# Performance work log

Measured on AMD Instinct MI355X. Metric: run time of the kernel, lower is better.

Reference implementation:

```python
import jax, jax.numpy as jnp
import numpy as np

NUM_HEADS = 16

def setup_inputs() -> dict:
    key = jax.random.key(0)
    k1, k2, k3 = jax.random.split(key, 3)
    B, T, C = 4, 2048, 2048
    x = jax.random.normal(k1, (B, T, C), dtype=jnp.float32)
    Wqkv = jax.random.normal(k2, (C, 3 * C), dtype=jnp.float32) * (C ** -0.5)
    bqkv = jnp.zeros((3 * C,), dtype=jnp.float32)
    Wproj = jax.random.normal(k3, (C, C), dtype=jnp.float32) * (C ** -0.5)
    bproj = jnp.zeros((C,), dtype=jnp.float32)
    return {"x": x, "Wqkv": Wqkv, "bqkv": bqkv, "Wproj": Wproj, "bproj": bproj}

def reference(x, Wqkv, bqkv, Wproj, bproj):
    B, T, C = x.shape
    H = NUM_HEADS
    D = C // H  # head_dim
    qkv = x @ Wqkv + bqkv                      # [B,T,3C]
    q, k, v = jnp.split(qkv, 3, axis=-1)
    # [B,T,C] -> [B,H,T,D]
    q = q.reshape(B, T, H, D).transpose(0, 2, 1, 3)
    k = k.reshape(B, T, H, D).transpose(0, 2, 1, 3)
    v = v.reshape(B, T, H, D).transpose(0, 2, 1, 3)
    scale = D ** -0.5
    scores = jnp.einsum('bhqd,bhkd->bhqk', q, k) * scale  # [B,H,T,T]
    causal = jnp.tril(jnp.ones((T, T), dtype=bool))
    scores = jnp.where(causal, scores, jnp.finfo(scores.dtype).min)
    attn = jax.nn.softmax(scores, axis=-1)
    out = jnp.einsum('bhqk,bhkd->bhqd', attn, v)           # [B,H,T,D]
    out = out.transpose(0, 2, 1, 3).reshape(B, T, C)
    return out @ Wproj + bproj
```

## Files before the change

### kernel.cpp

```cpp
#include <hip/hip_runtime.h>
#include <hip/hip_bf16.h>
#include <stdint.h>

typedef __attribute__((ext_vector_type(8))) short short8;
typedef __attribute__((ext_vector_type(4))) float f32x4;
typedef __attribute__((ext_vector_type(16))) float f32x16;
typedef __attribute__((ext_vector_type(2))) unsigned int uint2v;

__device__ __forceinline__ unsigned short f2bf(float f) {
  union { float f; unsigned int u; } v; v.f = f;
  unsigned int r = v.u + 0x7FFFu + ((v.u >> 16) & 1u);
  return (unsigned short)(r >> 16);
}

__device__ __forceinline__ unsigned int cvtpk(float lo, float hi) {
  unsigned int r;
  asm("v_cvt_pk_bf16_f32 %0, %1, %2" : "=v"(r) : "v"(lo), "v"(hi));
  return r;
}

#define GLOAD16(gsrc, ldst)                                                                  \
  __builtin_amdgcn_global_load_lds((const __attribute__((address_space(1))) void*)(gsrc),    \
                                   (__attribute__((address_space(3))) void*)(ldst), 16, 0, 0)

#define BAR() __builtin_amdgcn_s_barrier()
#define LGKM0() do { asm volatile("s_waitcnt lgkmcnt(0)" ::: "memory"); \
                     __builtin_amdgcn_sched_barrier(0); } while (0)
#define VMCNT0() asm volatile("s_waitcnt vmcnt(0)" ::: "memory")
#define PRIO(x) __builtin_amdgcn_s_setprio(x)
#define MFMA16(d, a, b) d = __builtin_amdgcn_mfma_f32_16x16x32_bf16(a, b, d, 0, 0, 0)

__global__ __launch_bounds__(256) void cast_bf16_kernel(const float* __restrict__ in,
                                                        unsigned short* __restrict__ out) {
  int i = blockIdx.x * 256 + threadIdx.x;
  float4 v = ((const float4*)in)[i];
  ushort4 o;
  o.x = f2bf(v.x); o.y = f2bf(v.y); o.z = f2bf(v.z); o.w = f2bf(v.w);
  ((ushort4*)out)[i] = o;
}

__global__ __launch_bounds__(256) void transpose_cast_kernel(const float* __restrict__ W,
                                                             unsigned short* __restrict__ Wt,
                                                             int K, int N) {
  __shared__ float tile[32][33];
  int n0 = blockIdx.x * 32, k0 = blockIdx.y * 32;
  int tx = threadIdx.x, ty = threadIdx.y;
#pragma unroll
  for (int j = 0; j < 32; j += 8)
    tile[ty + j][tx] = W[(size_t)(k0 + ty + j) * N + n0 + tx];
  __syncthreads();
#pragma unroll
  for (int j = 0; j < 32; j += 8)
    Wt[(size_t)(n0 + ty + j) * K + k0 + tx] = f2bf(tile[tx][ty + j]);
}

__device__ __forceinline__ void stageA128(const unsigned short* __restrict__ gp, int K,
                                          int kt, char* lds, int tid) {
#pragma unroll
  for (int it = 0; it < 4; ++it) {
    int li = it * 256 + tid;
    int r = li >> 3, c = li & 7;
    GLOAD16(gp + (size_t)r * K + kt * 64 + (c ^ (r & 7)) * 8, lds + li * 16);
  }
}
__device__ __forceinline__ void stageB256(const unsigned short* __restrict__ gp, int K,
                                          int kt, char* lds, int tid) {
#pragma unroll
  for (int it = 0; it < 8; ++it) {
    int li = it * 256 + tid;
    int r = li >> 3, c = li & 7;
    GLOAD16(gp + (size_t)r * K + kt * 64 + (c ^ (r & 7)) * 8, lds + li * 16);
  }
}

__device__ __forceinline__ void gemm128x256_mainloop(const unsigned short* __restrict__ Ap,
                                                     const unsigned short* __restrict__ Bp,
                                                     int K, int tid, char* smem,
                                                     f32x4 acc[4][8]) {
  char* sa = smem;
  char* sb = smem + 16384;
  const int KT = K >> 6;

  int wid = tid >> 6, lane = tid & 63;
  int wr = wid >> 1, wc = wid & 1;
  int lg = lane >> 4, l15 = lane & 15;
  int swz7 = l15 & 7;

#define LDA(m, kc) \
  (*(const short8*)((const unsigned short*)sa + (size_t)((wr * 64 + (m) * 16 + l15) * 64 + ((((kc) * 4 + lg) ^ swz7) * 8))))
#define LDB(n, kc) \
  (*(const short8*)((const unsigned short*)sb + (size_t)((wc * 128 + (n) * 16 + l15) * 64 + ((((kc) * 4 + lg) ^ swz7) * 8))))

  stageA128(Ap, K, 0, sa, tid);
  stageB256(Bp, K, 0, sb, tid);
  VMCNT0();
  BAR();

  for (int t = 0; t < KT; ++t) {
    short8 aq[4][2], bq[4][2];
#pragma unroll
    for (int m = 0; m < 4; ++m) { aq[m][0] = LDA(m, 0); aq[m][1] = LDA(m, 1); }
#pragma unroll
    for (int n = 0; n < 4; ++n) { bq[n][0] = LDB(n, 0); bq[n][1] = LDB(n, 1); }
    LGKM0();
    PRIO(1);
#pragma unroll
    for (int kc = 0; kc < 2; ++kc)
#pragma unroll
      for (int m = 0; m < 4; ++m)
#pragma unroll
        for (int n = 0; n < 4; ++n)
          MFMA16(acc[m][n], aq[m][kc], bq[n][kc]);
    PRIO(0);
#pragma unroll
    for (int n = 0; n < 4; ++n) { bq[n][0] = LDB(n + 4, 0); bq[n][1] = LDB(n + 4, 1); }
    LGKM0();
    PRIO(1);
#pragma unroll
    for (int kc = 0; kc < 2; ++kc)
#pragma unroll
      for (int m = 0; m < 4; ++m)
#pragma unroll
        for (int n = 0; n < 4; ++n)
          MFMA16(acc[m][n + 4], aq[m][kc], bq[n][kc]);
    PRIO(0);
    BAR();
    if (t + 1 < KT) {
      stageA128(Ap, K, t + 1, sa, tid);
      stageB256(Bp, K, t + 1, sb, tid);
      VMCNT0();
    }
    BAR();
  }
#undef LDA
#undef LDB
}

__global__ __launch_bounds__(256, 2) void gemm_qkv256_kernel(const unsigned short* __restrict__ A,
                                                             const unsigned short* __restrict__ Bt,
                                                             const float* __restrict__ bias,
                                                             unsigned short* __restrict__ qb,
                                                             unsigned short* __restrict__ kb,
                                                             unsigned short* __restrict__ vtb) {
  extern __shared__ char smem[];
  int wg = blockIdx.x;
  int xcd = wg & 7, idx = wg >> 3;
  int bn = xcd * 3 + idx % 3;
  int bm = idx / 3;
  int tid = threadIdx.x;

  f32x4 acc[4][8];
  f32x4 zero = {0.f, 0.f, 0.f, 0.f};
#pragma unroll
  for (int m = 0; m < 4; ++m)
#pragma unroll
    for (int n = 0; n < 8; ++n) acc[m][n] = zero;

  gemm128x256_mainloop(A + (size_t)bm * 128 * 2048, Bt + (size_t)bn * 256 * 2048, 2048, tid, smem, acc);

  const float QSCALE = (float)(0.08838834764831845 * 1.4426950408889634);
  int wid = tid >> 6, lane = tid & 63;
  int wr = wid >> 1, wc = wid & 1, lg = lane >> 4, l15 = lane & 15;

  if (bn >= 16) {
    int h0v = (bn - 16) * 2;
#pragma unroll
    for (int n = 0; n < 8; ++n) {
      int cl = wc * 128 + n * 16 + l15;
      float bv = bias[bn * 256 + cl];
#pragma unroll
      for (int m = 0; m < 4; ++m) {
        int rl = wr * 64 + m * 16 + lg * 4;
        unsigned int w0 = cvtpk(acc[m][n][0] + bv, acc[m][n][1] + bv);
        unsigned int w1 = cvtpk(acc[m][n][2] + bv, acc[m][n][3] + bv);
        uint2v pk = {w0, w1};
        *(uint2v*)(smem + cl * 256 + ((rl * 2) ^ ((cl & 7) << 4))) = pk;
      }
    }
    LGKM0();
    BAR();
    int b = (bm * 128) >> 11, t0 = (bm * 128) & 2047;
#pragma unroll
    for (int i = 0; i < 16; ++i) {
      int id = i * 256 + tid;
      int dloc = id >> 4, c = id & 15;
      short8 v = *(const short8*)(smem + dloc * 256 + ((c * 16) ^ ((dloc & 7) << 4)));
      int bh_ = b * 16 + h0v + (dloc >> 7);
      int d = dloc & 127;
      *(short8*)(vtb + ((size_t)bh_ * 128 + d) * 2048 + t0 + c * 8) = v;
    }
  } else {
    bool isq = (bn < 8);
#pragma unroll
    for (int n = 0; n < 8; ++n) {
      int cl = wc * 128 + n * 16 + l15;
      float bv = bias[bn * 256 + cl];
#pragma unroll
      for (int m = 0; m < 4; ++m) {
#pragma unroll
        for (int g = 0; g < 4; ++g) {
          int rl = wr * 64 + m * 16 + lg * 4 + g;
          float r = acc[m][n][g] + bv;
          if (isq) r *= QSCALE;
          *(unsigned short*)(smem + rl * 512 + ((cl * 2) ^ ((rl & 15) << 4))) = f2bf(r);
        }
      }
    }
    LGKM0();
    BAR();
    unsigned short* dst = isq ? qb : kb;
    int h0 = (bn & 7) * 2;
#pragma unroll
    for (int i = 0; i < 16; ++i) {
      int id = i * 256 + tid;
      int rl = id >> 5, c8 = id & 31;
      short8 v = *(const short8*)(smem + rl * 512 + ((c8 * 16) ^ ((rl & 15) << 4)));
      int row = bm * 128 + rl;
      int b = row >> 11, t = row & 2047;
      int h = h0 + (c8 >> 4);
      int d0 = (c8 & 15) * 8;
      *(short8*)(dst + ((size_t)(b * 16 + h) * 2048 + t) * 128 + d0) = v;
    }
  }
}

__global__ __launch_bounds__(256, 2) void gemm_proj256_kernel(const unsigned short* __restrict__ A,
                                                              const unsigned short* __restrict__ Bt,
                                                              const float* __restrict__ bias,
                                                              float* __restrict__ out) {
  extern __shared__ char smem[];
  int wg = blockIdx.x;
  int bm = wg >> 3, bn = wg & 7;
  int tid = threadIdx.x;

  f32x4 acc[4][8];
  f32x4 zero = {0.f, 0.f, 0.f, 0.f};
#pragma unroll
  for (int m = 0; m < 4; ++m)
#pragma unroll
    for (int n = 0; n < 8; ++n) acc[m][n] = zero;

  gemm128x256_mainloop(A + (size_t)bm * 128 * 2048, Bt + (size_t)bn * 256 * 2048, 2048, tid, smem, acc);

  int wid = tid >> 6, lane = tid & 63;
  int wr = wid >> 1, wc = wid & 1, lg = lane >> 4, l15 = lane & 15;
#pragma unroll
  for (int n = 0; n < 8; ++n) {
    int col = bn * 256 + wc * 128 + n * 16 + l15;
    float bv = bias[col];
#pragma unroll
    for (int m = 0; m < 4; ++m) {
#pragma unroll
      for (int g = 0; g < 4; ++g) {
        int row = bm * 128 + wr * 64 + m * 16 + lg * 4 + g;
        out[(size_t)row * 2048 + col] = acc[m][n][g] + bv;
      }
    }
  }
}

__global__ __launch_bounds__(512) void attn_kernel(const unsigned short* __restrict__ qb,
                                                   const unsigned short* __restrict__ kb,
                                                   const unsigned short* __restrict__ vtb,
                                                   unsigned short* __restrict__ ob) {
  extern __shared__ char asmem[];
  int bh = blockIdx.x;
  int pairi = blockIdx.y;
  int b = bh >> 4, h = bh & 15;
  int tid = threadIdx.x, wid = tid >> 6, lane = tid & 63;
  int l31 = lane & 31, hi = lane >> 5;

  const unsigned short* Q  = qb  + (size_t)bh * 2048 * 128;
  const unsigned short* K  = kb  + (size_t)bh * 2048 * 128;
  const unsigned short* Vt = vtb + (size_t)bh * 128 * 2048;

#pragma unroll 1
  for (int pass = 0; pass < 2; ++pass) {
    int qt = pass == 0 ? (7 - pairi) : pairi;
    int NT = 4 * qt + 4;
    int qbase = qt * 256 + wid * 32;
    int qrow = qbase + l31;

    short8 qf[8];
#pragma unroll
    for (int kc = 0; kc < 8; ++kc)
      qf[kc] = *(const short8*)(Q + (size_t)qrow * 128 + kc * 16 + hi * 8);

    f32x16 o0 = {}, o1 = {}, o2 = {}, o3 = {};
    float m_run = -1e30f, l_run = 0.f;

    {
      char* kb_ = asmem;
#pragma unroll
      for (int it = 0; it < 2; ++it) {
        int li = it * 512 + tid;
        int r = li >> 4, c = li & 15;
        GLOAD16(K + (size_t)r * 128 + (c ^ (r & 7)) * 8, kb_ + li * 16);
      }
#pragma unroll
      for (int it = 0; it < 2; ++it) {
        int li = it * 512 + tid;
        int r = li >> 3, c = li & 7;
        GLOAD16(Vt + (size_t)r * 2048 + (c ^ (r & 7)) * 8, kb_ + 16384 + li * 16);
      }
    }
    VMCNT0();
    BAR();

#pragma unroll 1
    for (int kt = 0; kt < NT; ++kt) {
      char* cb = asmem + ((kt & 1) << 15);
      if (kt + 1 < NT) {
        char* nb = asmem + (((kt + 1) & 1) << 15);
        int kt1 = kt + 1;
#pragma unroll
        for (int it = 0; it < 2; ++it) {
          int li = it * 512 + tid;
          int r = li >> 4, c = li & 15;
          GLOAD16(K + (size_t)(kt1 * 64 + r) * 128 + (c ^ (r & 7)) * 8, nb + li * 16);
        }
#pragma unroll
        for (int it = 0; it < 2; ++it) {
          int li = it * 512 + tid;
          int r = li >> 3, c = li & 7;
          GLOAD16(Vt + (size_t)r * 2048 + kt1 * 64 + (c ^ (r & 7)) * 8, nb + 16384 + li * 16);
        }
      }

      bool active = (kt * 64 <= qbase + 31);
      if (active) {
        const char* k_l = cb;
        const char* v_l = cb + 16384;

        f32x16 s0v = {}, s1v = {};
        PRIO(1);
#pragma unroll
        for (int kc = 0; kc < 8; ++kc) {
          int cg = kc * 2 + hi;
          int sw = l31 & 7;
          short8 kf0 = *(const short8*)(k_l + l31 * 256 + ((cg ^ sw) * 16));
          s0v = __builtin_amdgcn_mfma_f32_32x32x16_bf16(kf0, qf[kc], s0v, 0, 0, 0);
          short8 kf1 = *(const short8*)(k_l + (32 + l31) * 256 + ((cg ^ sw) * 16));
          s1v = __builtin_amdgcn_mfma_f32_32x32x16_bf16(kf1, qf[kc], s1v, 0, 0, 0);
        }
        PRIO(0);

        if (kt * 64 + 63 > qbase) {
          int kvb = kt * 64 + 4 * hi;
#pragma unroll
          for (int r = 0; r < 16; ++r) {
            int kv = kvb + (r & 3) + 8 * (r >> 2);
            if (kv > qrow) s0v[r] = -1e30f;
            if (kv + 32 > qrow) s1v[r] = -1e30f;
          }
        }

        float tmax[16];
#pragma unroll
        for (int i = 0; i < 16; ++i) tmax[i] = fmaxf(s0v[i], s1v[i]);
#pragma unroll
        for (int st = 8; st >= 1; st >>= 1)
#pragma unroll
          for (int i = 0; i < st; ++i) tmax[i] = fmaxf(tmax[i], tmax[i + st]);
        float pmax = fmaxf(tmax[0], __shfl_xor(tmax[0], 32));

        if (!__all(pmax <= m_run + 8.0f)) {
          float mn = fmaxf(m_run, pmax);
          float alpha = exp2f(m_run - mn);
          m_run = mn; l_run *= alpha;
          o0 *= alpha; o1 *= alpha; o2 *= alpha; o3 *= alpha;
        }

#pragma unroll
        for (int i = 0; i < 16; ++i) {
          s0v[i] = exp2f(s0v[i] - m_run);
          s1v[i] = exp2f(s1v[i] - m_run);
        }
        float tsum[16];
#pragma unroll
        for (int i = 0; i < 16; ++i) tsum[i] = s0v[i] + s1v[i];
#pragma unroll
        for (int st = 8; st >= 1; st >>= 1)
#pragma unroll
          for (int i = 0; i < st; ++i) tsum[i] += tsum[i + st];
        float rsum = tsum[0] + __shfl_xor(tsum[0], 32);
        l_run += rsum;

#define BUILD_PA(sv, base, out)                                                \
        {                                                                      \
          unsigned int a_ = cvtpk(sv[base + 0], sv[base + 1]);                 \
          unsigned int c_ = cvtpk(sv[base + 2], sv[base + 3]);                 \
          unsigned int b_ = cvtpk(sv[base + 4], sv[base + 5]);                 \
          unsigned int d_ = cvtpk(sv[base + 6], sv[base + 7]);                 \
          uint2v r0_ = __builtin_amdgcn_permlane32_swap(a_, b_, false, false); \
          uint2v r1_ = __builtin_amdgcn_permlane32_swap(c_, d_, false, false); \
          union { unsigned int u[4]; short8 v; } uu_;                          \
          uu_.u[0] = r0_[0]; uu_.u[1] = r1_[0]; uu_.u[2] = r0_[1]; uu_.u[3] = r1_[1]; \
          out = uu_.v;                                                         \
        }
        short8 pa0, pa1, pa2, pa3;
        BUILD_PA(s0v, 0, pa0);
        BUILD_PA(s0v, 8, pa1);
        BUILD_PA(s1v, 0, pa2);
        BUILD_PA(s1v, 8, pa3);
#undef BUILD_PA

        PRIO(1);
#define PV_STEP(ovar, dt)                                                          \
        {                                                                          \
          int rv_ = dt * 32 + l31;                                                 \
          const char* vb_ = v_l + rv_ * 128;                                       \
          int sw_ = rv_ & 7;                                                       \
          short8 v0_ = *(const short8*)(vb_ + (((0 + hi) ^ sw_) * 16));            \
          ovar = __builtin_amdgcn_mfma_f32_32x32x16_bf16(v0_, pa0, ovar, 0, 0, 0); \
          short8 v1_ = *(const short8*)(vb_ + (((2 + hi) ^ sw_) * 16));            \
          ovar = __builtin_amdgcn_mfma_f32_32x32x16_bf16(v1_, pa1, ovar, 0, 0, 0); \
          short8 v2_ = *(const short8*)(vb_ + (((4 + hi) ^ sw_) * 16));            \
          ovar = __builtin_amdgcn_mfma_f32_32x32x16_bf16(v2_, pa2, ovar, 0, 0, 0); \
          short8 v3_ = *(const short8*)(vb_ + (((6 + hi) ^ sw_) * 16));            \
          ovar = __builtin_amdgcn_mfma_f32_32x32x16_bf16(v3_, pa3, ovar, 0, 0, 0); \
        }
        PV_STEP(o0, 0)
        PV_STEP(o1, 1)
        PV_STEP(o2, 2)
        PV_STEP(o3, 3)
#undef PV_STEP
        PRIO(0);
      }

      VMCNT0();
      BAR();
    }

    float inv = 1.0f / l_run;
    size_t orow = (size_t)(b * 2048 + qt * 256 + wid * 32 + l31);
    unsigned short* ob_p = ob + orow * 2048 + h * 128;
#define STORE_DT(ovar, dt)                                                         \
    {                                                                              \
      _Pragma("unroll")                                                            \
      for (int rq = 0; rq < 4; ++rq) {                                             \
        unsigned int w0 = cvtpk(ovar[rq * 4 + 0] * inv, ovar[rq * 4 + 1] * inv);   \
        unsigned int w1 = cvtpk(ovar[rq * 4 + 2] * inv, ovar[rq * 4 + 3] * inv);   \
        uint2v st = {w0, w1};                                                      \
        *(uint2v*)(ob_p + dt * 32 + rq * 8 + 4 * hi) = st;                         \
      }                                                                            \
    }
    STORE_DT(o0, 0)
    STORE_DT(o1, 1)
    STORE_DT(o2, 2)
    STORE_DT(o3, 3)
#undef STORE_DT
  }
}

extern "C" void kernel_launch(void* const* d_in, const int* in_sizes, int n_in,
                              void* d_out, int out_size, void* d_ws, size_t ws_size,
                              hipStream_t stream) {
  const float* x     = (const float*)d_in[0];
  const float* Wqkv  = (const float*)d_in[1];
  const float* bqkv  = (const float*)d_in[2];
  const float* Wproj = (const float*)d_in[3];
  const float* bproj = (const float*)d_in[4];
  float* out = (float*)d_out;

  char* ws = (char*)d_ws;
  unsigned short* x_bf   = (unsigned short*)ws;
  unsigned short* wqkvt  = (unsigned short*)(ws + 33554432);
  unsigned short* wprojt = (unsigned short*)(ws + 33554432 + 25165824);
  unsigned short* qb     = (unsigned short*)(ws + 67108864);
  unsigned short* kb     = (unsigned short*)(ws + 100663296);
  unsigned short* vtb    = (unsigned short*)(ws + 134217728);

  (void)hipFuncSetAttribute((const void*)gemm_qkv256_kernel,
                            hipFuncAttributeMaxDynamicSharedMemorySize, 65536);
  (void)hipFuncSetAttribute((const void*)gemm_proj256_kernel,
                            hipFuncAttributeMaxDynamicSharedMemorySize, 65536);
  (void)hipFuncSetAttribute((const void*)attn_kernel,
                            hipFuncAttributeMaxDynamicSharedMemorySize, 65536);

  cast_bf16_kernel<<<16384, 256, 0, stream>>>(x, x_bf);
  transpose_cast_kernel<<<dim3(192, 64), dim3(32, 8), 0, stream>>>(Wqkv, wqkvt, 2048, 6144);
  transpose_cast_kernel<<<dim3(64, 64), dim3(32, 8), 0, stream>>>(Wproj, wprojt, 2048, 2048);
  gemm_qkv256_kernel<<<1536, 256, 65536, stream>>>(x_bf, wqkvt, bqkv, qb, kb, vtb);
  attn_kernel<<<dim3(64, 4), 512, 65536, stream>>>(qb, kb, vtb, x_bf );
  gemm_proj256_kernel<<<512, 256, 65536, stream>>>(x_bf, wprojt, bproj, out);
}
```

Baseline: 397.7 us.

## Rewrite projection GEMM as 256x256 tile with 8 waves and interleaved prefetch

```diff
diff --git a/kernel.cpp b/kernel.cpp
--- a/kernel.cpp
+++ b/kernel.cpp
@@ -24,9 +24,12 @@
                                    (__attribute__((address_space(3))) void*)(ldst), 16, 0, 0)
 
 #define BAR() __builtin_amdgcn_s_barrier()
-#define LGKM0() do { asm volatile("s_waitcnt lgkmcnt(0)" ::: "memory"); \
-                     __builtin_amdgcn_sched_barrier(0); } while (0)
+#define LGKMC(n) do { asm volatile("s_waitcnt lgkmcnt(" #n ")" ::: "memory"); \
+                      __builtin_amdgcn_sched_barrier(0); } while (0)
+#define LGKM0() LGKMC(0)
 #define VMCNT0() asm volatile("s_waitcnt vmcnt(0)" ::: "memory")
+#define VMCNT8() do { asm volatile("s_waitcnt vmcnt(8)" ::: "memory"); \
+                      __builtin_amdgcn_sched_barrier(0); } while (0)
 #define PRIO(x) __builtin_amdgcn_s_setprio(x)
 #define MFMA16(d, a, b) d = __builtin_amdgcn_mfma_f32_16x16x32_bf16(a, b, d, 0, 0, 0)
 
@@ -134,6 +137,118 @@
   }
 #undef LDA
 #undef LDB
+}
+
+__device__ __forceinline__ void stage_half(const unsigned short* __restrict__ gp, int K,
+                                           int kt, int half, char* lds_mat, int tid) {
+#pragma unroll
+  for (int it = 0; it < 2; ++it) {
+    int li = half * 1024 + it * 512 + tid;
+    int r = li >> 3, c = li & 7;
+    int cs = c ^ (r & 7);
+    GLOAD16(gp + (size_t)r * K + kt * 64 + cs * 8, lds_mat + li * 16);
+  }
+}
+
+__device__ __forceinline__ void gemm256sq_mainloop(const unsigned short* __restrict__ Ap,
+                                                   const unsigned short* __restrict__ Bp,
+                                                   int K, int tid, char* smem,
+                                                   f32x4 acc[8][4]) {
+  char* sa = smem;
+  char* sb = smem + 65536;
+  const int KT = K >> 6;
+
+  int wid = tid >> 6, lane = tid & 63;
+  int wr = wid >> 2, wc = wid & 3;
+  int lg = lane >> 4, l15 = lane & 15;
+  int swz7 = l15 & 7;
+
+#define LDA2(ab, m, kc) \
+  (*(const short8*)((const unsigned short*)(ab) + (size_t)((wr * 128 + (m) * 16 + l15) * 64 + ((((kc) * 4 + lg) ^ swz7) * 8))))
+#define LDB2(bb, n, kc) \
+  (*(const short8*)((const unsigned short*)(bb) + (size_t)((wc * 64 + (n) * 16 + l15) * 64 + ((((kc) * 4 + lg) ^ swz7) * 8))))
+
+  stage_half(Bp, K, 0, 0, sb, tid);
+  stage_half(Bp, K, 0, 1, sb, tid);
+  stage_half(Ap, K, 0, 0, sa, tid);
+  stage_half(Ap, K, 0, 1, sa, tid);
+  stage_half(Bp, K, 1, 0, sb + 32768, tid);
+  stage_half(Bp, K, 1, 1, sb + 32768, tid);
+  stage_half(Ap, K, 1, 0, sa + 32768, tid);
+  stage_half(Ap, K, 1, 1, sa + 32768, tid);
+  VMCNT8();
+  BAR();
+
+  for (int t = 0; t < KT; ++t) {
+    int p = t & 1;
+    const char* ab = sa + p * 32768;
+    const char* bb = sb + p * 32768;
+    int kt2 = (t + 2 < KT) ? t + 2 : KT - 1;
+
+    short8 bq01[2][2], bq23[2][2], aq[4][2], aq2[4][2];
+#pragma unroll
+    for (int n = 0; n < 2; ++n) { bq01[n][0] = LDB2(bb, n, 0); bq01[n][1] = LDB2(bb, n, 1); }
+#pragma unroll
+    for (int m = 0; m < 4; ++m) { aq[m][0] = LDA2(ab, m, 0); aq[m][1] = LDA2(ab, m, 1); }
+#pragma unroll
+    for (int n = 0; n < 2; ++n) { bq23[n][0] = LDB2(bb, n + 2, 0); bq23[n][1] = LDB2(bb, n + 2, 1); }
+#pragma unroll
+    for (int m = 0; m < 4; ++m) { aq2[m][0] = LDA2(ab, m + 4, 0); aq2[m][1] = LDA2(ab, m + 4, 1); }
+
+    LGKMC(12);
+    PRIO(1);
+#pragma unroll
+    for (int kc = 0; kc < 2; ++kc)
+#pragma unroll
+      for (int m = 0; m < 4; ++m)
+#pragma unroll
+        for (int n = 0; n < 2; ++n)
+          MFMA16(acc[m][n], aq[m][kc], bq01[n][kc]);
+    PRIO(0);
+
+    LGKMC(8);
+    BAR();
+    stage_half(Bp, K, kt2, 0, sb + p * 32768, tid);
+    stage_half(Bp, K, kt2, 1, sb + p * 32768, tid);
+
+    PRIO(1);
+#pragma unroll
+    for (int kc = 0; kc < 2; ++kc)
+#pragma unroll
+      for (int m = 0; m < 4; ++m)
+#pragma unroll
+        for (int n = 0; n < 2; ++n)
+          MFMA16(acc[m][n + 2], aq[m][kc], bq23[n][kc]);
+    PRIO(0);
+
+    LGKMC(0);
+    PRIO(1);
+#pragma unroll
+    for (int kc = 0; kc < 2; ++kc)
+#pragma unroll
+      for (int m = 0; m < 4; ++m)
+#pragma unroll
+        for (int n = 0; n < 2; ++n)
+          MFMA16(acc[m + 4][n + 2], aq2[m][kc], bq23[n][kc]);
+    PRIO(0);
+
+    BAR();
+    stage_half(Ap, K, kt2, 0, sa + p * 32768, tid);
+    stage_half(Ap, K, kt2, 1, sa + p * 32768, tid);
+    PRIO(1);
+#pragma unroll
+    for (int kc = 0; kc < 2; ++kc)
+#pragma unroll
+      for (int m = 0; m < 4; ++m)
+#pragma unroll
+        for (int n = 0; n < 2; ++n)
+          MFMA16(acc[m + 4][n], aq2[m][kc], bq01[n][kc]);
+    PRIO(0);
+    VMCNT8();
+    BAR();
+  }
+#undef LDA2
+#undef LDB2
 }
 
 __global__ __launch_bounds__(256, 2) void gemm_qkv256_kernel(const unsigned short* __restrict__ A,
@@ -224,7 +339,7 @@
   }
 }
 
-__global__ __launch_bounds__(256, 2) void gemm_proj256_kernel(const unsigned short* __restrict__ A,
+__global__ __launch_bounds__(512, 2) void gemm_proj256_kernel(const unsigned short* __restrict__ A,
                                                               const unsigned short* __restrict__ Bt,
                                                               const float* __restrict__ bias,
                                                               float* __restrict__ out) {
@@ -233,26 +348,26 @@
   int bm = wg >> 3, bn = wg & 7;
   int tid = threadIdx.x;
 
-  f32x4 acc[4][8];
+  f32x4 acc[8][4];
   f32x4 zero = {0.f, 0.f, 0.f, 0.f};
 #pragma unroll
-  for (int m = 0; m < 4; ++m)
-#pragma unroll
-    for (int n = 0; n < 8; ++n) acc[m][n] = zero;
-
-  gemm128x256_mainloop(A + (size_t)bm * 128 * 2048, Bt + (size_t)bn * 256 * 2048, 2048, tid, smem, acc);
+  for (int m = 0; m < 8; ++m)
+#pragma unroll
+    for (int n = 0; n < 4; ++n) acc[m][n] = zero;
+
+  gemm256sq_mainloop(A + (size_t)bm * 256 * 2048, Bt + (size_t)bn * 256 * 2048, 2048, tid, smem, acc);
 
   int wid = tid >> 6, lane = tid & 63;
-  int wr = wid >> 1, wc = wid & 1, lg = lane >> 4, l15 = lane & 15;
-#pragma unroll
-  for (int n = 0; n < 8; ++n) {
-    int col = bn * 256 + wc * 128 + n * 16 + l15;
+  int wr = wid >> 2, wc = wid & 3, lg = lane >> 4, l15 = lane & 15;
+#pragma unroll
+  for (int n = 0; n < 4; ++n) {
+    int col = bn * 256 + wc * 64 + n * 16 + l15;
     float bv = bias[col];
 #pragma unroll
-    for (int m = 0; m < 4; ++m) {
+    for (int m = 0; m < 8; ++m) {
 #pragma unroll
       for (int g = 0; g < 4; ++g) {
-        int row = bm * 128 + wr * 64 + m * 16 + lg * 4 + g;
+        int row = bm * 256 + wr * 128 + m * 16 + lg * 4 + g;
         out[(size_t)row * 2048 + col] = acc[m][n][g] + bv;
       }
     }
@@ -474,7 +589,7 @@
   (void)hipFuncSetAttribute((const void*)gemm_qkv256_kernel,
                             hipFuncAttributeMaxDynamicSharedMemorySize, 65536);
   (void)hipFuncSetAttribute((const void*)gemm_proj256_kernel,
-                            hipFuncAttributeMaxDynamicSharedMemorySize, 65536);
+                            hipFuncAttributeMaxDynamicSharedMemorySize, 131072);
   (void)hipFuncSetAttribute((const void*)attn_kernel,
                             hipFuncAttributeMaxDynamicSharedMemorySize, 65536);
 
@@ -483,5 +598,5 @@
   transpose_cast_kernel<<<dim3(64, 64), dim3(32, 8), 0, stream>>>(Wproj, wprojt, 2048, 2048);
   gemm_qkv256_kernel<<<1536, 256, 65536, stream>>>(x_bf, wqkvt, bqkv, qb, kb, vtb);
   attn_kernel<<<dim3(64, 4), 512, 65536, stream>>>(qb, kb, vtb, x_bf );
-  gemm_proj256_kernel<<<512, 256, 65536, stream>>>(x_bf, wprojt, bproj, out);
-}
+  gemm_proj256_kernel<<<256, 512, 131072, stream>>>(x_bf, wprojt, bproj, out);
+}
```

Measured after the change: 392.5 us. Within noise of the previous version (-1.3%).
